# Performance work log

Measured on AMD Instinct MI355X. Metric: run time of the kernel, lower is better.

## Reference

```python
import jax, jax.numpy as jnp
import numpy as np

B, C_IN, C_OUT, H, MAXN = 128, 32, 32, 4096, 6


def setup_inputs() -> dict:
    key = jax.random.key(0)
    ks = jax.random.split(key, 6)
    x = jax.random.normal(ks[0], (B, C_IN, H), dtype=jnp.float32)
    weight = jax.random.normal(ks[1], (C_OUT, C_IN, MAXN + 1), dtype=jnp.float32) * 0.05
    bias = jax.random.normal(ks[2], (C_OUT,), dtype=jnp.float32) * 0.05
    gamma = jnp.ones((C_OUT,), dtype=jnp.float32)
    beta = jnp.zeros((C_OUT,), dtype=jnp.float32)
    # hex neighbor table; -1 marks invalid (boundary) neighbors
    neighbors = jax.random.randint(ks[3], (H, MAXN), -1, H, dtype=jnp.int64)
    return {"x": x, "weight": weight, "bias": bias, "gamma": gamma,
            "beta": beta, "neighbors": neighbors, "groups": 1}


def reference(x, weight, bias, gamma, beta, neighbors, groups):
    Bsz, Cin, Hn = x.shape
    Cout, _, K = weight.shape  # K = total_inputs = max_neighbors + 1
    G = groups
    # global std normalization (torch std: unbiased, ddof=1)
    x = x / (jnp.std(x, ddof=1) + 1e-5)
    valid = (neighbors >= 0)                      # [H, K-1]
    idx = jnp.clip(neighbors, 0, None)
    nbr = x[:, :, idx] * valid.astype(x.dtype)[None, None]   # [B,C,H,K-1]
    allv = jnp.concatenate([x[..., None], nbr], axis=3)      # [B,C,H,K]
    allv = allv.reshape(Bsz, G, Cin // G, Hn, K)
    w = weight.reshape(G, Cout // G, Cin // G, K)
    out = jnp.einsum('bgihk,goik->bgoh', allv, w).reshape(Bsz, Cout, Hn)
    total_valid = valid.sum(axis=1).astype(out.dtype)[None, None] + 1.0  # [1,1,H]
    out = out / (total_valid + 1e-6)
    out = out + bias[None, :, None]
    # BatchNorm1d in training mode: per-channel over (batch, hex), biased var
    mean = out.mean(axis=(0, 2), keepdims=True)
    var = out.var(axis=(0, 2), keepdims=True)
    out = gamma[None, :, None] * (out - mean) * jax.lax.rsqrt(var + 1e-5) + beta[None, :, None]
    return out
```

## Files before the change

kernel.cpp:

```cpp
#include <hip/hip_runtime.h>
#include <stdint.h>
#include <stddef.h>

#define BSZ 128
#define CIN 32
#define COUT 32
#define HN 4096
#define K7 7
#define NTOT (BSZ*CIN*HN)
#define NBH  (BSZ*HN)

typedef __attribute__((ext_vector_type(8))) short short8;
typedef __attribute__((ext_vector_type(4))) float f32x4;

#define WS_XT   0
#define WS_WT   33554432
#define WS_NBR  33568768
#define WS_INVD 33699840
#define WS_OSTP 33716224
#define WS_OST  33781760

__device__ __forceinline__ unsigned short f32_to_bf16(float f){
    union { float f; uint32_t u; } v; v.f = f;
    uint32_t u = v.u;
    return (unsigned short)((u + 0x7FFFu + ((u >> 16) & 1u)) >> 16);
}

__global__ void kinit(const int* __restrict__ nbr,
                      const float* __restrict__ w,
                      int* __restrict__ nbr_pack,
                      float* __restrict__ invd,
                      unsigned short* __restrict__ wt,
                      float* __restrict__ ostatp){
    int t = threadIdx.x;
    if (blockIdx.x < 16){
        int h = blockIdx.x*256 + t;
        #pragma unroll
        for (int j = 0; j < 4; j++) ostatp[h*4 + j] = 0.0f;
        int cnt = 0;
        int pk[8];
        #pragma unroll
        for (int j = 0; j < 6; j++){
            int iv = nbr[h*6 + j];
            if (iv >= HN) iv = HN - 1;
            if (iv >= 0) cnt++; else iv = -1;
            pk[j] = iv;
        }
        pk[6] = cnt; pk[7] = 0;
        #pragma unroll
        for (int j = 0; j < 8; j++) nbr_pack[h*8 + j] = pk[j];
        invd[h] = 1.0f / ((float)cnt + 1.0f + 1e-6f);
    } else {
        for (int i = t; i < COUT*K7*CIN; i += 256){
            int o  = i / (K7*CIN);
            int kk = (i / CIN) % K7;
            int c  = i % CIN;
            wt[i] = f32_to_bf16(w[(o*CIN + c)*K7 + kk]);
        }
    }
}

__global__ void ktrans(const float* __restrict__ x,
                       unsigned short* __restrict__ xt){
    __shared__ float tile[32][260];
    int b  = blockIdx.x >> 4;
    int h0 = (blockIdx.x & 15) << 8;
    int t  = threadIdx.x;
    #pragma unroll
    for (int l = 0; l < 8; l++){
        int linear = l*256 + t;
        int c  = linear >> 6;
        int h4 = linear & 63;
        float4 v = *(const float4*)(x + ((size_t)(b*CIN + c))*HN + h0 + h4*4);
        *(float4*)&tile[c][h4*4] = v;
    }
    __syncthreads();
    int cg = (t & 3) * 8;
    int hw = t >> 2;
    #pragma unroll
    for (int r = 0; r < 4; r++){
        int h = r*64 + hw;
        alignas(16) unsigned short tmp[8];
        #pragma unroll
        for (int j = 0; j < 8; j++) tmp[j] = f32_to_bf16(tile[cg + j][h]);
        *(uint4*)(xt + ((size_t)(b*HN + h0 + h))*32 + cg) = *(const uint4*)tmp;
    }
}

__device__ __forceinline__ void gather7(short8* dst, const unsigned short* xb,
                                        int selfrow, int4 na, int4 nb, int quad){
    const short8 zero8 = {0,0,0,0,0,0,0,0};
    dst[0] = *(const short8*)(xb + (size_t)selfrow*CIN + quad*8);
    int rows[6] = {na.x, na.y, na.z, na.w, nb.x, nb.y};
    #pragma unroll
    for (int k = 0; k < 6; k++){
        int r  = rows[k];
        int rc = r < 0 ? 0 : r;
        dst[k+1] = *(const short8*)(xb + (size_t)rc*CIN + quad*8);
        if (r < 0) dst[k+1] = zero8;
    }
}

template<bool APPLY>
__global__ __launch_bounds__(256) void kconv_t(
    const unsigned short* __restrict__ xt,
    const unsigned short* __restrict__ wt,
    const int* __restrict__ nbrp,
    const float* __restrict__ invd,
    const float* __restrict__ ostat,
    const float* __restrict__ gamma,
    const float* __restrict__ beta,
    float* __restrict__ out,
    float* __restrict__ ostatp)
{
    int lane = threadIdx.x & 63;
    int wv   = threadIdx.x >> 6;
    int n    = lane & 15;
    int quad = lane >> 4;
    int xcd  = blockIdx.x & 7;
    int j    = blockIdx.x >> 3;
    int b    = xcd*16 + (j >> 4);
    int hbase= ((j & 15)*4 + wv) * 64;

    short8 af[2][K7];
    #pragma unroll
    for (int mt = 0; mt < 2; mt++){
        int o = n + 16*mt;
        #pragma unroll
        for (int kk = 0; kk < K7; kk++)
            af[mt][kk] = *(const short8*)(wt + (size_t)(o*K7 + kk)*CIN + quad*8);
    }

    float sc8[2][4], sh8[2][4];
    if (APPLY){
        #pragma unroll
        for (int mt = 0; mt < 2; mt++)
            #pragma unroll
            for (int r = 0; r < 4; r++){
                int o = mt*16 + quad*4 + r;
                float mean = ostat[o]      * (1.0f/(float)NBH);
                float var  = ostat[32 + o] * (1.0f/(float)NBH) - mean*mean;
                float s = gamma[o] * rsqrtf(var + 1e-5f);
                sc8[mt][r] = s;
                sh8[mt][r] = beta[o] - mean*s;
            }
    }

    float sacc[8]  = {0,0,0,0,0,0,0,0};
    float sacc2[8] = {0,0,0,0,0,0,0,0};
    const unsigned short* xb = xt + (size_t)b*HN*CIN;
    int hn0 = hbase + n;

    int4 na[2], nb[2]; float iv[2];
    short8 buf[2][K7];
    na[0] = *(const int4*)(nbrp + hn0*8);
    nb[0] = *(const int4*)(nbrp + hn0*8 + 4);
    iv[0] = invd[hn0];
    na[1] = *(const int4*)(nbrp + (hn0+16)*8);
    nb[1] = *(const int4*)(nbrp + (hn0+16)*8 + 4);
    iv[1] = invd[hn0+16];
    gather7(buf[0], xb, hn0, na[0], nb[0], quad);

    #pragma unroll
    for (int it = 0; it < 4; it++){
        int s = it & 1, o2 = s ^ 1;
        float idv = iv[s];
        if (it + 1 < 4)
            gather7(buf[o2], xb, hn0 + (it+1)*16, na[o2], nb[o2], quad);
        if (it + 2 < 4){
            na[s] = *(const int4*)(nbrp + (hn0 + (it+2)*16)*8);
            nb[s] = *(const int4*)(nbrp + (hn0 + (it+2)*16)*8 + 4);
            iv[s] = invd[hn0 + (it+2)*16];
        }
        f32x4 acc0 = {0.f,0.f,0.f,0.f};
        f32x4 acc1 = {0.f,0.f,0.f,0.f};
        #pragma unroll
        for (int kk = 0; kk < K7; kk++){
            acc0 = __builtin_amdgcn_mfma_f32_16x16x32_bf16(af[0][kk], buf[s][kk], acc0, 0, 0, 0);
            acc1 = __builtin_amdgcn_mfma_f32_16x16x32_bf16(af[1][kk], buf[s][kk], acc1, 0, 0, 0);
        }
        int hc = hbase + it*16 + n;
        #pragma unroll
        for (int mt = 0; mt < 2; mt++){
            f32x4 a = mt ? acc1 : acc0;
            #pragma unroll
            for (int r = 0; r < 4; r++){
                float v = a[r]*idv;
                if (APPLY){
                    int o = mt*16 + quad*4 + r;
                    out[((size_t)(b*COUT + o))*HN + hc] = v*sc8[mt][r] + sh8[mt][r];
                } else {
                    sacc[mt*4 + r]  += v;
                    sacc2[mt*4 + r] += v*v;
                }
            }
        }
    }

    if (!APPLY){
        #pragma unroll
        for (int bit = 1; bit < 16; bit <<= 1){
            #pragma unroll
            for (int i = 0; i < 8; i++){
                sacc[i]  += __shfl_xor(sacc[i],  bit);
                sacc2[i] += __shfl_xor(sacc2[i], bit);
            }
        }
        if (n == 0){
            int slot = blockIdx.x & 255;
            #pragma unroll
            for (int mt = 0; mt < 2; mt++)
                #pragma unroll
                for (int r = 0; r < 4; r++){
                    int o = mt*16 + quad*4 + r;
                    atomicAdd(&ostatp[slot*64 + o],      sacc[mt*4 + r]);
                    atomicAdd(&ostatp[slot*64 + 32 + o], sacc2[mt*4 + r]);
                }
        }
    }
}

__global__ void kred(const float* __restrict__ ostatp,
                     float* __restrict__ ostat){
    __shared__ float part[4][64];
    int t = threadIdx.x;
    int a = t & 63;
    int g = t >> 6;
    float s = 0.0f;
    #pragma unroll
    for (int j = 0; j < 64; j++)
        s += ostatp[(g*64 + j)*64 + a];
    part[g][a] = s;
    __syncthreads();
    if (t < 64)
        ostat[t] = part[0][t] + part[1][t] + part[2][t] + part[3][t];
}

extern "C" void kernel_launch(void* const* d_in, const int* in_sizes, int n_in,
                              void* d_out, int out_size, void* d_ws, size_t ws_size,
                              hipStream_t stream) {
    const float* x      = (const float*)d_in[0];
    const float* weight = (const float*)d_in[1];
    const float* gamma  = (const float*)d_in[3];
    const float* beta   = (const float*)d_in[4];
    const int*   nbr    = (const int*)d_in[5];

    char* ws = (char*)d_ws;
    unsigned short* xt    = (unsigned short*)(ws + WS_XT);
    unsigned short* wt    = (unsigned short*)(ws + WS_WT);
    int*            nbrp  = (int*)(ws + WS_NBR);
    float*          invd  = (float*)(ws + WS_INVD);
    float*          ostatp= (float*)(ws + WS_OSTP);
    float*          ostat = (float*)(ws + WS_OST);
    float*          out   = (float*)d_out;

    kinit        <<<17,   256, 0, stream>>>(nbr, weight, nbrp, invd, wt, ostatp);
    ktrans       <<<2048, 256, 0, stream>>>(x, xt);
    kconv_t<false><<<2048, 256, 0, stream>>>(xt, wt, nbrp, invd, nullptr, nullptr, nullptr, nullptr, ostatp);
    kred         <<<1,    256, 0, stream>>>(ostatp, ostat);
    kconv_t<true> <<<2048, 256, 0, stream>>>(xt, wt, nbrp, invd, ostat, gamma, beta, out, nullptr);
}
```

Measured before the change: 191.2 us.

## Fuse conv stats and BN apply into one persistent kernel with grid barrier

Replaces the two conv passes and the reduction kernel with a single kernel of 1024 blocks. Each block computes its conv outputs once, keeps them as bf16 in shared memory, and publishes channel sums. A software grid barrier on global flags then lets every block reduce the stats and apply batch norm from the held values. This removes the recomputation of the gather and MFMA work and two kernel launches. The cost is an occupancy requirement (all 1024 blocks must be resident for the barrier to finish), a timeout escape that could yield wrong stats, and bf16 rounding of intermediate outputs.

New measurement: 598.5 us. 213% more time.

```diff
diff --git a/kernel.cpp b/kernel.cpp
--- a/kernel.cpp
+++ b/kernel.cpp
@@ -18,12 +18,16 @@
 #define WS_NBR  33568768
 #define WS_INVD 33699840
 #define WS_OSTP 33716224
-#define WS_OST  33781760
+#define WS_BAR  33732608
 
 __device__ __forceinline__ unsigned short f32_to_bf16(float f){
     union { float f; uint32_t u; } v; v.f = f;
     uint32_t u = v.u;
     return (unsigned short)((u + 0x7FFFu + ((u >> 16) & 1u)) >> 16);
+}
+__device__ __forceinline__ float bf16_to_f32(unsigned short h){
+    union { uint32_t u; float f; } v; v.u = ((uint32_t)h) << 16;
+    return v.f;
 }
 
 __global__ void kinit(const int* __restrict__ nbr,
@@ -31,12 +35,13 @@
                       int* __restrict__ nbr_pack,
                       float* __restrict__ invd,
                       unsigned short* __restrict__ wt,
-                      float* __restrict__ ostatp){
+                      float* __restrict__ ostatp,
+                      int* __restrict__ bar){
     int t = threadIdx.x;
     if (blockIdx.x < 16){
         int h = blockIdx.x*256 + t;
-        #pragma unroll
-        for (int j = 0; j < 4; j++) ostatp[h*4 + j] = 0.0f;
+        ostatp[h] = 0.0f;
+        if (h < 1024) bar[h] = 0;
         int cnt = 0;
         int pk[8];
         #pragma unroll
@@ -101,26 +106,30 @@
     }
 }
 
-template<bool APPLY>
-__global__ __launch_bounds__(256) void kconv_t(
+__global__ __launch_bounds__(256, 4) void kfused(
     const unsigned short* __restrict__ xt,
     const unsigned short* __restrict__ wt,
     const int* __restrict__ nbrp,
     const float* __restrict__ invd,
-    const float* __restrict__ ostat,
     const float* __restrict__ gamma,
     const float* __restrict__ beta,
     float* __restrict__ out,
-    float* __restrict__ ostatp)
+    float* __restrict__ ostatp,
+    int* __restrict__ bar)
 {
-    int lane = threadIdx.x & 63;
-    int wv   = threadIdx.x >> 6;
+    __shared__ uint4 held[8*256];
+    __shared__ float part[4][64];
+    __shared__ float scsh[64];
+
+    int t    = threadIdx.x;
+    int lane = t & 63;
+    int wv   = t >> 6;
     int n    = lane & 15;
     int quad = lane >> 4;
     int xcd  = blockIdx.x & 7;
     int j    = blockIdx.x >> 3;
-    int b    = xcd*16 + (j >> 4);
-    int hbase= ((j & 15)*4 + wv) * 64;
+    int b    = xcd*16 + (j >> 3);
+    int hbase= (j & 7)*512 + wv*128;
 
     short8 af[2][K7];
     #pragma unroll
@@ -131,109 +140,133 @@
             af[mt][kk] = *(const short8*)(wt + (size_t)(o*K7 + kk)*CIN + quad*8);
     }
 
-    float sc8[2][4], sh8[2][4];
-    if (APPLY){
-        #pragma unroll
-        for (int mt = 0; mt < 2; mt++)
+    const unsigned short* xb = xt + (size_t)b*HN*CIN;
+
+    #pragma unroll 2
+    for (int it = 0; it < 8; it++){
+        int hc = hbase + it*16 + n;
+        int4 na = *(const int4*)(nbrp + hc*8);
+        int4 nb = *(const int4*)(nbrp + hc*8 + 4);
+        float idv = invd[hc];
+        short8 bfr[K7];
+        gather7(bfr, xb, hc, na, nb, quad);
+        f32x4 acc0 = {0.f,0.f,0.f,0.f};
+        f32x4 acc1 = {0.f,0.f,0.f,0.f};
+        #pragma unroll
+        for (int kk = 0; kk < K7; kk++){
+            acc0 = __builtin_amdgcn_mfma_f32_16x16x32_bf16(af[0][kk], bfr[kk], acc0, 0, 0, 0);
+            acc1 = __builtin_amdgcn_mfma_f32_16x16x32_bf16(af[1][kk], bfr[kk], acc1, 0, 0, 0);
+        }
+        uint32_t w_[4];
+        #pragma unroll
+        for (int p = 0; p < 2; p++){
+            f32x4 a = p ? acc1 : acc0;
+            w_[p*2]   = (uint32_t)f32_to_bf16(a[0]*idv) | ((uint32_t)f32_to_bf16(a[1]*idv) << 16);
+            w_[p*2+1] = (uint32_t)f32_to_bf16(a[2]*idv) | ((uint32_t)f32_to_bf16(a[3]*idv) << 16);
+        }
+        uint4 pk; pk.x = w_[0]; pk.y = w_[1]; pk.z = w_[2]; pk.w = w_[3];
+        held[it*256 + t] = pk;
+    }
+
+    float sacc[8]  = {0,0,0,0,0,0,0,0};
+    float sacc2[8] = {0,0,0,0,0,0,0,0};
+    #pragma unroll
+    for (int it = 0; it < 8; it++){
+        uint4 pk = held[it*256 + t];
+        uint32_t w_[4] = {pk.x, pk.y, pk.z, pk.w};
+        #pragma unroll
+        for (int i = 0; i < 8; i++){
+            float v = bf16_to_f32((unsigned short)((w_[i>>1] >> ((i&1)*16)) & 0xFFFF));
+            sacc[i]  += v;
+            sacc2[i] += v*v;
+        }
+    }
+    #pragma unroll
+    for (int bit = 1; bit < 16; bit <<= 1){
+        #pragma unroll
+        for (int i = 0; i < 8; i++){
+            sacc[i]  += __shfl_xor(sacc[i],  bit);
+            sacc2[i] += __shfl_xor(sacc2[i], bit);
+        }
+    }
+    if (n == 0){
+        int slot = blockIdx.x & 63;
+        #pragma unroll
+        for (int p = 0; p < 2; p++)
             #pragma unroll
             for (int r = 0; r < 4; r++){
-                int o = mt*16 + quad*4 + r;
-                float mean = ostat[o]      * (1.0f/(float)NBH);
-                float var  = ostat[32 + o] * (1.0f/(float)NBH) - mean*mean;
-                float s = gamma[o] * rsqrtf(var + 1e-5f);
-                sc8[mt][r] = s;
-                sh8[mt][r] = beta[o] - mean*s;
+                int o = p*16 + quad*4 + r;
+                atomicAdd(&ostatp[slot*64 + o],      sacc[p*4 + r]);
+                atomicAdd(&ostatp[slot*64 + 32 + o], sacc2[p*4 + r]);
             }
     }
 
-    float sacc[8]  = {0,0,0,0,0,0,0,0};
-    float sacc2[8] = {0,0,0,0,0,0,0,0};
-    const unsigned short* xb = xt + (size_t)b*HN*CIN;
-    int hn0 = hbase + n;
-
-    int4 na[2], nb[2]; float iv[2];
-    short8 buf[2][K7];
-    na[0] = *(const int4*)(nbrp + hn0*8);
-    nb[0] = *(const int4*)(nbrp + hn0*8 + 4);
-    iv[0] = invd[hn0];
-    na[1] = *(const int4*)(nbrp + (hn0+16)*8);
-    nb[1] = *(const int4*)(nbrp + (hn0+16)*8 + 4);
-    iv[1] = invd[hn0+16];
-    gather7(buf[0], xb, hn0, na[0], nb[0], quad);
-
-    #pragma unroll
-    for (int it = 0; it < 4; it++){
-        int s = it & 1, o2 = s ^ 1;
-        float idv = iv[s];
-        if (it + 1 < 4)
-            gather7(buf[o2], xb, hn0 + (it+1)*16, na[o2], nb[o2], quad);
-        if (it + 2 < 4){
-            na[s] = *(const int4*)(nbrp + (hn0 + (it+2)*16)*8);
-            nb[s] = *(const int4*)(nbrp + (hn0 + (it+2)*16)*8 + 4);
-            iv[s] = invd[hn0 + (it+2)*16];
-        }
-        f32x4 acc0 = {0.f,0.f,0.f,0.f};
-        f32x4 acc1 = {0.f,0.f,0.f,0.f};
-        #pragma unroll
-        for (int kk = 0; kk < K7; kk++){
-            acc0 = __builtin_amdgcn_mfma_f32_16x16x32_bf16(af[0][kk], buf[s][kk], acc0, 0, 0, 0);
-            acc1 = __builtin_amdgcn_mfma_f32_16x16x32_bf16(af[1][kk], buf[s][kk], acc1, 0, 0, 0);
-        }
+    __syncthreads();
+    if (t == 0){
+        __threadfence();
+        __hip_atomic_store(&bar[blockIdx.x], 1, __ATOMIC_RELEASE, __HIP_MEMORY_SCOPE_AGENT);
+    }
+    {
+        const int* s0 = bar + t*4;
+        long tries = 0;
+        for (;;){
+            int c = __hip_atomic_load(s0+0, __ATOMIC_ACQUIRE, __HIP_MEMORY_SCOPE_AGENT)
+                  + __hip_atomic_load(s0+1, __ATOMIC_ACQUIRE, __HIP_MEMORY_SCOPE_AGENT)
+                  + __hip_atomic_load(s0+2, __ATOMIC_ACQUIRE, __HIP_MEMORY_SCOPE_AGENT)
+                  + __hip_atomic_load(s0+3, __ATOMIC_ACQUIRE, __HIP_MEMORY_SCOPE_AGENT);
+            if (c == 4) break;
+            if (++tries > (1L<<24)) break;
+            __builtin_amdgcn_s_sleep(8);
+        }
+        __threadfence();
+        __syncthreads();
+    }
+
+    {
+        int a = t & 63, g = t >> 6;
+        float s = 0.0f;
+        #pragma unroll
+        for (int jj = 0; jj < 16; jj++)
+            s += __hip_atomic_load(&ostatp[(g*16 + jj)*64 + a],
+                                   __ATOMIC_RELAXED, __HIP_MEMORY_SCOPE_AGENT);
+        part[g][a] = s;
+        __syncthreads();
+        if (t < 64) part[0][t] = part[0][t] + part[1][t] + part[2][t] + part[3][t];
+        __syncthreads();
+        if (t < 32){
+            float mean = part[0][t]      * (1.0f/(float)NBH);
+            float var  = part[0][32 + t] * (1.0f/(float)NBH) - mean*mean;
+            float sc = gamma[t] * rsqrtf(var + 1e-5f);
+            scsh[t] = sc;
+            scsh[32 + t] = beta[t] - mean*sc;
+        }
+        __syncthreads();
+    }
+    float sA[8], sB[8];
+    #pragma unroll
+    for (int p = 0; p < 2; p++)
+        #pragma unroll
+        for (int r = 0; r < 4; r++){
+            int o = p*16 + quad*4 + r;
+            sA[p*4 + r] = scsh[o];
+            sB[p*4 + r] = scsh[32 + o];
+        }
+
+    #pragma unroll 2
+    for (int it = 0; it < 8; it++){
         int hc = hbase + it*16 + n;
-        #pragma unroll
-        for (int mt = 0; mt < 2; mt++){
-            f32x4 a = mt ? acc1 : acc0;
+        uint4 pk = held[it*256 + t];
+        uint32_t w_[4] = {pk.x, pk.y, pk.z, pk.w};
+        #pragma unroll
+        for (int p = 0; p < 2; p++)
             #pragma unroll
             for (int r = 0; r < 4; r++){
-                float v = a[r]*idv;
-                if (APPLY){
-                    int o = mt*16 + quad*4 + r;
-                    out[((size_t)(b*COUT + o))*HN + hc] = v*sc8[mt][r] + sh8[mt][r];
-                } else {
-                    sacc[mt*4 + r]  += v;
-                    sacc2[mt*4 + r] += v*v;
-                }
+                int i = p*4 + r;
+                float v = bf16_to_f32((unsigned short)((w_[i>>1] >> ((i&1)*16)) & 0xFFFF));
+                int o = p*16 + quad*4 + r;
+                out[((size_t)(b*COUT + o))*HN + hc] = v*sA[i] + sB[i];
             }
-        }
-    }
-
-    if (!APPLY){
-        #pragma unroll
-        for (int bit = 1; bit < 16; bit <<= 1){
-            #pragma unroll
-            for (int i = 0; i < 8; i++){
-                sacc[i]  += __shfl_xor(sacc[i],  bit);
-                sacc2[i] += __shfl_xor(sacc2[i], bit);
-            }
-        }
-        if (n == 0){
-            int slot = blockIdx.x & 255;
-            #pragma unroll
-            for (int mt = 0; mt < 2; mt++)
-                #pragma unroll
-                for (int r = 0; r < 4; r++){
-                    int o = mt*16 + quad*4 + r;
-                    atomicAdd(&ostatp[slot*64 + o],      sacc[mt*4 + r]);
-                    atomicAdd(&ostatp[slot*64 + 32 + o], sacc2[mt*4 + r]);
-                }
-        }
-    }
-}
-
-__global__ void kred(const float* __restrict__ ostatp,
-                     float* __restrict__ ostat){
-    __shared__ float part[4][64];
-    int t = threadIdx.x;
-    int a = t & 63;
-    int g = t >> 6;
-    float s = 0.0f;
-    #pragma unroll
-    for (int j = 0; j < 64; j++)
-        s += ostatp[(g*64 + j)*64 + a];
-    part[g][a] = s;
-    __syncthreads();
-    if (t < 64)
-        ostat[t] = part[0][t] + part[1][t] + part[2][t] + part[3][t];
+    }
 }
 
 extern "C" void kernel_launch(void* const* d_in, const int* in_sizes, int n_in,
@@ -251,12 +284,10 @@
     int*            nbrp  = (int*)(ws + WS_NBR);
     float*          invd  = (float*)(ws + WS_INVD);
     float*          ostatp= (float*)(ws + WS_OSTP);
-    float*          ostat = (float*)(ws + WS_OST);
+    int*            bar   = (int*)(ws + WS_BAR);
     float*          out   = (float*)d_out;
 
-    kinit        <<<17,   256, 0, stream>>>(nbr, weight, nbrp, invd, wt, ostatp);
-    ktrans       <<<2048, 256, 0, stream>>>(x, xt);
-    kconv_t<false><<<2048, 256, 0, stream>>>(xt, wt, nbrp, invd, nullptr, nullptr, nullptr, nullptr, ostatp);
-    kred         <<<1,    256, 0, stream>>>(ostatp, ostat);
-    kconv_t<true> <<<2048, 256, 0, stream>>>(xt, wt, nbrp, invd, ostat, gamma, beta, out, nullptr);
-}
+    kinit <<<17,   256, 0, stream>>>(nbr, weight, nbrp, invd, wt, ostatp, bar);
+    ktrans<<<2048, 256, 0, stream>>>(x, xt);
+    kfused<<<1024, 256, 0, stream>>>(xt, wt, nbrp, invd, gamma, beta, out, ostatp, bar);
+}
```
